# Kernel tuning notes

Hardware: AMD Instinct MI355X
Metric: run time of the kernel (lower is better)

Reference implementation:

```python
import jax, jax.numpy as jnp
import numpy as np

BITS = 4
GROUPSIZE = 128
INF = 4096
OUTF = 4096
PACK = 32 // BITS  # 8 nibbles per int32


def _dequant(qweight, qzeros, scales):
    # qweight: [INF//PACK, OUTF] int32, qzeros: [n_groups, OUTF//PACK] int32
    shifts = (jnp.arange(PACK, dtype=jnp.int32) * BITS)
    # unpack weights: each int32 row holds PACK consecutive input rows
    w = (qweight[:, None, :] >> shifts[None, :, None]) & 15        # [512, 8, 4096]
    w = w.reshape(-1, GROUPSIZE, OUTF)                              # [n_groups, groupsize, OUTF]
    # unpack zeros: each int32 col holds PACK consecutive output cols
    z = ((qzeros[:, :, None] >> shifts[None, None, :]) & 15) + 1   # [n_groups, 512, 8]
    z = z.reshape(z.shape[0], 1, -1)                                # [n_groups, 1, OUTF]
    W = scales[:, None, :] * (w - z).astype(scales.dtype)           # per-group dequant
    return W.reshape(INF, OUTF)


def setup_inputs() -> dict:
    key = jax.random.key(0)
    k1, k2, k3, k4, k5 = jax.random.split(key, 5)
    x = jax.random.normal(k1, (8, 512, INF), dtype=jnp.float32)
    qweight = jax.random.randint(k2, (INF // PACK, OUTF), 0, 2147483647, dtype=jnp.int32)
    n_groups = INF // GROUPSIZE
    qzeros = jax.random.randint(k3, (n_groups, OUTF // PACK), 0, 2147483647, dtype=jnp.int32)
    scales = jax.random.uniform(k4, (n_groups, OUTF), dtype=jnp.float32) * 0.01 + 0.001
    bias = jax.random.normal(k5, (OUTF,), dtype=jnp.float32) * 0.01
    return {"x": x, "qweight": qweight, "qzeros": qzeros, "scales": scales, "bias": bias}


def reference(x, qweight, qzeros, scales, bias):
    W = _dequant(qweight, qzeros, scales)        # [INF, OUTF] fp32
    out = jnp.matmul(x, W.astype(x.dtype)) + bias
    return out
```

## Files before the change

### kernel.cpp

```cpp
#include <hip/hip_runtime.h>
#include <hip/hip_bf16.h>


#define K_DIM 4096
#define N_DIM 4096
#define M_DIM 4096
#define BM 256
#define BN 256
#define BK 64
#define NGROUPS 32

typedef __attribute__((ext_vector_type(8))) short s8v;
typedef __attribute__((ext_vector_type(4))) float f4v;
typedef __attribute__((ext_vector_type(4))) unsigned int u4v;
typedef __attribute__((ext_vector_type(2))) unsigned int u2v;
typedef __attribute__((ext_vector_type(4))) float float4v;

typedef __attribute__((address_space(3))) void LDSV;
typedef const __attribute__((address_space(1))) void GLBV;

__device__ __forceinline__ void glds16(const void* g, void* l) {
    __builtin_amdgcn_global_load_lds((GLBV*)g, (LDSV*)l, 16, 0, 0);
}

__device__ __forceinline__ unsigned int bf16rne(float f) {
    unsigned int b = __float_as_uint(f);
    return (b + 0x7FFFu + ((b >> 16) & 1u)) >> 16;
}

__global__ __launch_bounds__(256) void castx(const float* __restrict__ x,
                                             unsigned short* __restrict__ xh,
                                             int n4) {
    int i0 = blockIdx.x * 256 + threadIdx.x;
    int st = gridDim.x * 256;
    for (int i = i0; i < n4; i += st) {
        float4v v = ((const float4v*)x)[i];
        unsigned int h[4];
#pragma unroll
        for (int j = 0; j < 4; j++) {
            unsigned int b = __float_as_uint(v[j]);
            h[j] = (b + 0x7FFFu + ((b >> 16) & 1u)) & 0xFFFF0000u;
        }
        u2v o = {(h[0] >> 16) | h[1], (h[2] >> 16) | h[3]};
        ((u2v*)xh)[i] = o;
    }
}

__global__ __launch_bounds__(256) void dequantW(const int* __restrict__ qw,
                                                const int* __restrict__ qz,
                                                const float* __restrict__ scales,
                                                unsigned short* __restrict__ wt) {
    __shared__ __align__(16) unsigned short T[256 * 64];
    const int b = blockIdx.x;
    const int kkb = b & 63;
    const int nb = b >> 6;
    const int tid = threadIdx.x;
    const int n = nb * 256 + tid;
    const int g = kkb >> 1;
    const float s = scales[g * N_DIM + n];
    const int zp1 = ((qz[g * 512 + (n >> 3)] >> ((n & 7) * 4)) & 15) + 1;

    char* Tb = (char*)T;
#pragma unroll
    for (int r = 0; r < 8; r++) {
        const unsigned int q = (unsigned int)qw[(kkb * 8 + r) * N_DIM + n];
        unsigned int hw[8];
#pragma unroll
        for (int j = 0; j < 8; j++) {
            float v = s * (float)((int)((q >> (4 * j)) & 15u) - zp1);
            hw[j] = bf16rne(v);
        }
        u4v d = {hw[0] | (hw[1] << 16), hw[2] | (hw[3] << 16),
                 hw[4] | (hw[5] << 16), hw[6] | (hw[7] << 16)};
        *(u4v*)(Tb + tid * 128 + ((r * 16) ^ ((tid & 7) << 4))) = d;
    }
    __syncthreads();
#pragma unroll
    for (int p = 0; p < 8; p++) {
        const int nl = p * 32 + (tid >> 3);
        const int c = tid & 7;
        u4v d = *(const u4v*)(Tb + nl * 128 + ((c * 16) ^ ((nl & 7) << 4)));
        *(u4v*)(wt + (size_t)(nb * 256 + nl) * K_DIM + kkb * 64 + c * 8) = d;
    }
}

#define STAGE_A(BUF, H, T)                                                    \
    {                                                                         \
        _Pragma("unroll") for (int j = 0; j < 2; j++) {                       \
            const int s_ = 2 * wid + j;                                       \
            const int rA = (s_ < 8) ? ((H) * 64 + s_ * 8)                     \
                                    : (128 + (H) * 64 + (s_ - 8) * 8);        \
            glds16(xh + (size_t)(bm + rA + (lane >> 3)) * K_DIM + (T)*BK +    \
                       aswz,                                                  \
                   &LDS_[BUF][0][(H)*8192 + s_ * 512]);                       \
        }                                                                     \
    }
#define STAGE_B(BUF, H, T)                                                    \
    {                                                                         \
        _Pragma("unroll") for (int j = 0; j < 2; j++) {                       \
            const int s_ = 2 * wid + j;                                       \
            const int cB = ((s_ >> 2) << 6) + ((H) << 5) + ((s_ & 3) << 3);   \
            glds16(wt + (size_t)(bn + cB + (lane >> 3)) * K_DIM + (T)*BK +    \
                       aswz,                                                  \
                   &LDS_[BUF][1][(H)*8192 + s_ * 512]);                       \
        }                                                                     \
    }
#define VM6 asm volatile("s_waitcnt vmcnt(6)" ::: "memory");
#define VM0 asm volatile("s_waitcnt vmcnt(0)" ::: "memory");
#define NOP ;

#define PHASE(BUF, QM, QN, STAGE_CODE, WAIT_CODE)                             \
    {                                                                         \
        if ((QN) == 0) {                                                      \
            const char* Ab = (const char*)&LDS_[BUF][0][(QM)*8192];           \
            _Pragma("unroll") for (int mi = 0; mi < 4; mi++) {                \
                const int pos = wr * 64 + mi * 16 + frow;                     \
                const int ro = pos * 128;                                     \
                const int sw = (pos & 7) << 4;                                \
                afr[mi][0] = *(const s8v*)(Ab + ro + (fk16 ^ sw));            \
                afr[mi][1] = *(const s8v*)(Ab + ro + ((64 | fk16) ^ sw));     \
            }                                                                 \
        }                                                                     \
        if ((QM) == 0) {                                                      \
            const char* Bb = (const char*)&LDS_[BUF][1][(QN)*8192];           \
            _Pragma("unroll") for (int ni = 0; ni < 2; ni++) {                \
                const int pos = wc * 32 + ni * 16 + frow;                     \
                const int ro = pos * 128;                                     \
                const int sw = (pos & 7) << 4;                                \
                bfr[QN][ni][0] = *(const s8v*)(Bb + ro + (fk16 ^ sw));        \
                bfr[QN][ni][1] = *(const s8v*)(Bb + ro + ((64 | fk16) ^ sw)); \
            }                                                                 \
        }                                                                     \
        STAGE_CODE                                                            \
        __builtin_amdgcn_s_barrier();                                         \
        asm volatile("s_waitcnt lgkmcnt(0)" ::: "memory");                    \
        __builtin_amdgcn_s_setprio(1);                                        \
        _Pragma("unroll") for (int mi = 0; mi < 4; mi++)                      \
            _Pragma("unroll") for (int ni = 0; ni < 2; ni++) {                \
            acc[(QM)*4 + mi][(QN)*2 + ni] =                                   \
                __builtin_amdgcn_mfma_f32_16x16x32_bf16(                      \
                    afr[mi][0], bfr[QN][ni][0],                               \
                    acc[(QM)*4 + mi][(QN)*2 + ni], 0, 0, 0);                  \
            acc[(QM)*4 + mi][(QN)*2 + ni] =                                   \
                __builtin_amdgcn_mfma_f32_16x16x32_bf16(                      \
                    afr[mi][1], bfr[QN][ni][1],                               \
                    acc[(QM)*4 + mi][(QN)*2 + ni], 0, 0, 0);                  \
        }                                                                     \
        __builtin_amdgcn_s_setprio(0);                                        \
        WAIT_CODE                                                             \
        __builtin_amdgcn_s_barrier();                                         \
    }

__global__ __launch_bounds__(512, 2) void gemm8(
    const unsigned short* __restrict__ xh, const unsigned short* __restrict__ wt,
    const float* __restrict__ bias, float* __restrict__ out) {
    __shared__ __align__(16) unsigned short LDS_[2][2][16384];

    const int tid = threadIdx.x;
    const int lane = tid & 63;
    const int wid = tid >> 6;
    const int wr = wid >> 2;
    const int wc = wid & 3;

    const int bid = blockIdx.x;
    const int wg = ((bid & 7) << 5) + (bid >> 3);
    const int bm = (wg >> 4) << 8;
    const int bn = (wg & 15) << 8;

    const int frow = lane & 15;
    const int fk16 = (lane >> 4) << 4;
    const int aswz = ((lane & 7) ^ (lane >> 3)) << 3;

    const f4v z4 = {0.f, 0.f, 0.f, 0.f};
    f4v acc[8][4];
#pragma unroll
    for (int i = 0; i < 8; i++)
#pragma unroll
        for (int j = 0; j < 4; j++) acc[i][j] = z4;

    s8v afr[4][2];
    s8v bfr[2][2][2];

    STAGE_A(0, 0, 0)
    STAGE_A(0, 1, 0)
    STAGE_B(0, 0, 0)
    STAGE_B(0, 1, 0)
    STAGE_A(1, 0, 1)
    STAGE_B(1, 0, 1)
    STAGE_B(1, 1, 1)
    VM6
    __builtin_amdgcn_s_barrier();

#pragma unroll 1
    for (int i = 0; i < 31; ++i) {
        const int t1 = 2 * i + 1, t2 = 2 * i + 2, t3 = 2 * i + 3;
        PHASE(0, 0, 0, STAGE_A(1, 1, t1), NOP)
        PHASE(0, 0, 1, STAGE_A(0, 0, t2), NOP)
        PHASE(0, 1, 0, STAGE_B(0, 0, t2), NOP)
        PHASE(0, 1, 1, STAGE_B(0, 1, t2), VM6)
        PHASE(1, 0, 0, STAGE_A(0, 1, t2), NOP)
        PHASE(1, 0, 1, STAGE_A(1, 0, t3), NOP)
        PHASE(1, 1, 0, STAGE_B(1, 0, t3), NOP)
        PHASE(1, 1, 1, STAGE_B(1, 1, t3), VM6)
    }
    PHASE(0, 0, 0, STAGE_A(1, 1, 63), NOP)
    PHASE(0, 0, 1, NOP, NOP)
    PHASE(0, 1, 0, NOP, NOP)
    PHASE(0, 1, 1, NOP, VM0)
    PHASE(1, 0, 0, NOP, NOP)
    PHASE(1, 0, 1, NOP, NOP)
    PHASE(1, 1, 0, NOP, NOP)
    PHASE(1, 1, 1, NOP, NOP)

    const int row0 = bm + wr * 128 + ((lane >> 4) << 2);
    const int col0 = bn + wc * 64 + frow;
#pragma unroll
    for (int n = 0; n < 4; n++) {
        const int cn = col0 + (n >> 1) * 32 + (n & 1) * 16;
        const float bv = bias[cn];
#pragma unroll
        for (int m = 0; m < 8; m++) {
            const int rm = row0 + (m >> 2) * 64 + (m & 3) * 16;
            f4v v = acc[m][n];
#pragma unroll
            for (int r2 = 0; r2 < 4; r2++)
                out[(size_t)(rm + r2) * N_DIM + cn] = v[r2] + bv;
        }
    }
}

__global__ __launch_bounds__(256) void naive_q4(
    const float* __restrict__ x, const int* __restrict__ qw,
    const int* __restrict__ qz, const float* __restrict__ scales,
    const float* __restrict__ bias, float* __restrict__ out) {
    const int n = (blockIdx.x & 63) * 64 + (threadIdx.x & 63);
    const int m = (blockIdx.x >> 6) * 4 + (threadIdx.x >> 6);
    const float* xr = x + (size_t)m * K_DIM;
    float acc = 0.f;
    for (int g = 0; g < NGROUPS; ++g) {
        const float s = scales[g * N_DIM + n];
        const int z = ((qz[g * 512 + (n >> 3)] >> ((n & 7) * 4)) & 15) + 1;
        float gs = 0.f;
        for (int kk = 0; kk < 16; ++kk) {
            const int q = qw[(g * 16 + kk) * N_DIM + n];
            const float* xp = xr + g * 128 + kk * 8;
#pragma unroll
            for (int j = 0; j < 8; j++)
                gs += xp[j] * (float)(((q >> (4 * j)) & 15) - z);
        }
        acc += s * gs;
    }
    out[(size_t)m * N_DIM + n] = acc + bias[n];
}

extern "C" void kernel_launch(void* const* d_in, const int* in_sizes, int n_in,
                              void* d_out, int out_size, void* d_ws,
                              size_t ws_size, hipStream_t stream) {
    const float* x = (const float*)d_in[0];
    const int* qw = (const int*)d_in[1];
    const int* qz = (const int*)d_in[2];
    const float* sc = (const float*)d_in[3];
    const float* bias = (const float*)d_in[4];
    float* out = (float*)d_out;

    const size_t nel = (size_t)M_DIM * K_DIM;
    const size_t need = nel * 2 * sizeof(unsigned short);
    if (ws_size >= need) {
        unsigned short* xh = (unsigned short*)d_ws;
        unsigned short* wtp = xh + nel;
        castx<<<2048, 256, 0, stream>>>(x, xh, (int)(nel / 4));
        dequantW<<<64 * 16, 256, 0, stream>>>(qw, qz, sc, wtp);
        gemm8<<<(M_DIM / BM) * (N_DIM / BN), 512, 0, stream>>>(xh, wtp, bias,
                                                               out);
    } else {
        naive_q4<<<(M_DIM / 4) * (N_DIM / 64), 256, 0, stream>>>(x, qw, qz, sc,
                                                                 bias, out);
    }
}
```

Before: 248.4 us.

## Fuse cast and dequant prep kernels; split GEMM phases to overlap LDS reads with MFMA

The x-to-bf16 cast and the weight dequantisation are merged into a single launch that gives them disjoint block ranges, saving one kernel launch and letting the two passes run at the same time. The GEMM main loop is rebuilt from 8 uniform phases into a per-buffer pass. A-fragment LDS reads are split into halves and interleaved with MFMA batches, so the second half's reads hide behind the first half's compute. This brings more barriers and scheduling changes that may perturb the compiler's instruction ordering and register pressure.

After: 246.2 us. Within noise of the previous version (-0.9%).

```diff
diff --git a/kernel.cpp b/kernel.cpp
--- a/kernel.cpp
+++ b/kernel.cpp
@@ -28,33 +28,34 @@
     return (b + 0x7FFFu + ((b >> 16) & 1u)) >> 16;
 }
 
-__global__ __launch_bounds__(256) void castx(const float* __restrict__ x,
-                                             unsigned short* __restrict__ xh,
-                                             int n4) {
-    int i0 = blockIdx.x * 256 + threadIdx.x;
-    int st = gridDim.x * 256;
-    for (int i = i0; i < n4; i += st) {
-        float4v v = ((const float4v*)x)[i];
-        unsigned int h[4];
-#pragma unroll
-        for (int j = 0; j < 4; j++) {
-            unsigned int b = __float_as_uint(v[j]);
-            h[j] = (b + 0x7FFFu + ((b >> 16) & 1u)) & 0xFFFF0000u;
-        }
-        u2v o = {(h[0] >> 16) | h[1], (h[2] >> 16) | h[3]};
-        ((u2v*)xh)[i] = o;
-    }
-}
-
-__global__ __launch_bounds__(256) void dequantW(const int* __restrict__ qw,
-                                                const int* __restrict__ qz,
-                                                const float* __restrict__ scales,
-                                                unsigned short* __restrict__ wt) {
+__global__ __launch_bounds__(256) void prep(const float* __restrict__ x,
+                                            unsigned short* __restrict__ xh,
+                                            const int* __restrict__ qw,
+                                            const int* __restrict__ qz,
+                                            const float* __restrict__ scales,
+                                            unsigned short* __restrict__ wt) {
     __shared__ __align__(16) unsigned short T[256 * 64];
+    const int tid = threadIdx.x;
+    if (blockIdx.x >= 1024) {
+        const int n4 = (M_DIM * K_DIM) / 4;
+        int i0 = (blockIdx.x - 1024) * 256 + tid;
+        const int st = 2048 * 256;
+        for (int i = i0; i < n4; i += st) {
+            float4v v = ((const float4v*)x)[i];
+            unsigned int h[4];
+#pragma unroll
+            for (int j = 0; j < 4; j++) {
+                unsigned int b = __float_as_uint(v[j]);
+                h[j] = (b + 0x7FFFu + ((b >> 16) & 1u)) & 0xFFFF0000u;
+            }
+            u2v o = {(h[0] >> 16) | h[1], (h[2] >> 16) | h[3]};
+            ((u2v*)xh)[i] = o;
+        }
+        return;
+    }
     const int b = blockIdx.x;
     const int kkb = b & 63;
     const int nb = b >> 6;
-    const int tid = threadIdx.x;
     const int n = nb * 256 + tid;
     const int g = kkb >> 1;
     const float s = scales[g * N_DIM + n];
@@ -105,51 +106,72 @@
                    &LDS_[BUF][1][(H)*8192 + s_ * 512]);                       \
         }                                                                     \
     }
+#define RD_A2(BUF, QM, MI0)                                                   \
+    {                                                                         \
+        const char* Ab = (const char*)&LDS_[BUF][0][(QM)*8192];               \
+        _Pragma("unroll") for (int mi = (MI0); mi < (MI0) + 2; mi++) {        \
+            const int pos = wr * 64 + mi * 16 + frow;                         \
+            const int ro = pos * 128;                                         \
+            const int sw = (pos & 7) << 4;                                    \
+            afr[mi][0] = *(const s8v*)(Ab + ro + (fk16 ^ sw));                \
+            afr[mi][1] = *(const s8v*)(Ab + ro + ((64 | fk16) ^ sw));         \
+        }                                                                     \
+    }
+#define RD_B(BUF, H)                                                          \
+    {                                                                         \
+        const char* Bb = (const char*)&LDS_[BUF][1][(H)*8192];                \
+        _Pragma("unroll") for (int ni = 0; ni < 2; ni++) {                    \
+            const int pos = wc * 32 + ni * 16 + frow;                         \
+            const int ro = pos * 128;                                         \
+            const int sw = (pos & 7) << 4;                                    \
+            bfr[H][ni][0] = *(const s8v*)(Bb + ro + (fk16 ^ sw));             \
+            bfr[H][ni][1] = *(const s8v*)(Bb + ro + ((64 | fk16) ^ sw));      \
+        }                                                                     \
+    }
+#define MM2(MI0, QM, QN)                                                      \
+    _Pragma("unroll") for (int mi = (MI0); mi < (MI0) + 2; mi++)              \
+        _Pragma("unroll") for (int ni = 0; ni < 2; ni++) {                    \
+        acc[(QM)*4 + mi][(QN)*2 + ni] =                                       \
+            __builtin_amdgcn_mfma_f32_16x16x32_bf16(                          \
+                afr[mi][0], bfr[QN][ni][0], acc[(QM)*4 + mi][(QN)*2 + ni], 0, \
+                0, 0);                                                        \
+        acc[(QM)*4 + mi][(QN)*2 + ni] =                                       \
+            __builtin_amdgcn_mfma_f32_16x16x32_bf16(                          \
+                afr[mi][1], bfr[QN][ni][1], acc[(QM)*4 + mi][(QN)*2 + ni], 0, \
+                0, 0);                                                        \
+    }
 #define VM6 asm volatile("s_waitcnt vmcnt(6)" ::: "memory");
 #define VM0 asm volatile("s_waitcnt vmcnt(0)" ::: "memory");
-#define NOP ;
-
-#define PHASE(BUF, QM, QN, STAGE_CODE, WAIT_CODE)                             \
-    {                                                                         \
-        if ((QN) == 0) {                                                      \
-            const char* Ab = (const char*)&LDS_[BUF][0][(QM)*8192];           \
-            _Pragma("unroll") for (int mi = 0; mi < 4; mi++) {                \
-                const int pos = wr * 64 + mi * 16 + frow;                     \
-                const int ro = pos * 128;                                     \
-                const int sw = (pos & 7) << 4;                                \
-                afr[mi][0] = *(const s8v*)(Ab + ro + (fk16 ^ sw));            \
-                afr[mi][1] = *(const s8v*)(Ab + ro + ((64 | fk16) ^ sw));     \
-            }                                                                 \
-        }                                                                     \
-        if ((QM) == 0) {                                                      \
-            const char* Bb = (const char*)&LDS_[BUF][1][(QN)*8192];           \
-            _Pragma("unroll") for (int ni = 0; ni < 2; ni++) {                \
-                const int pos = wc * 32 + ni * 16 + frow;                     \
-                const int ro = pos * 128;                                     \
-                const int sw = (pos & 7) << 4;                                \
-                bfr[QN][ni][0] = *(const s8v*)(Bb + ro + (fk16 ^ sw));        \
-                bfr[QN][ni][1] = *(const s8v*)(Bb + ro + ((64 | fk16) ^ sw)); \
-            }                                                                 \
-        }                                                                     \
-        STAGE_CODE                                                            \
-        __builtin_amdgcn_s_barrier();                                         \
-        asm volatile("s_waitcnt lgkmcnt(0)" ::: "memory");                    \
-        __builtin_amdgcn_s_setprio(1);                                        \
-        _Pragma("unroll") for (int mi = 0; mi < 4; mi++)                      \
-            _Pragma("unroll") for (int ni = 0; ni < 2; ni++) {                \
-            acc[(QM)*4 + mi][(QN)*2 + ni] =                                   \
-                __builtin_amdgcn_mfma_f32_16x16x32_bf16(                      \
-                    afr[mi][0], bfr[QN][ni][0],                               \
-                    acc[(QM)*4 + mi][(QN)*2 + ni], 0, 0, 0);                  \
-            acc[(QM)*4 + mi][(QN)*2 + ni] =                                   \
-                __builtin_amdgcn_mfma_f32_16x16x32_bf16(                      \
-                    afr[mi][1], bfr[QN][ni][1],                               \
-                    acc[(QM)*4 + mi][(QN)*2 + ni], 0, 0, 0);                  \
-        }                                                                     \
-        __builtin_amdgcn_s_setprio(0);                                        \
-        WAIT_CODE                                                             \
-        __builtin_amdgcn_s_barrier();                                         \
-    }
+#define BAR __builtin_amdgcn_s_barrier();
+#define PRIO1 __builtin_amdgcn_s_setprio(1);
+#define PRIO0 __builtin_amdgcn_s_setprio(0);
+
+#define BUFPASS(BUF, SC1, SC2, SC3, SC4, W4)                                  \
+    RD_A2(BUF, 0, 0) RD_B(BUF, 0)                                             \
+    SC1                                                                       \
+    BAR                                                                       \
+    PRIO1 MM2(0, 0, 0) PRIO0                                                  \
+    RD_A2(BUF, 0, 2) RD_B(BUF, 1)                                             \
+    PRIO1 MM2(2, 0, 0) PRIO0                                                  \
+    BAR                                                                       \
+    SC2                                                                       \
+    BAR                                                                       \
+    PRIO1 MM2(0, 0, 1) MM2(2, 0, 1) PRIO0                                     \
+    BAR                                                                       \
+    RD_A2(BUF, 1, 0)                                                          \
+    SC3                                                                       \
+    BAR                                                                       \
+    PRIO1 MM2(0, 1, 0) PRIO0                                                  \
+    RD_A2(BUF, 1, 2)                                                          \
+    PRIO1 MM2(2, 1, 0) PRIO0                                                  \
+    BAR                                                                       \
+    SC4                                                                       \
+    BAR                                                                       \
+    PRIO1 MM2(0, 1, 1) MM2(2, 1, 1) PRIO0                                     \
+    W4                                                                        \
+    BAR
+
+#define SNOP ;
 
 __global__ __launch_bounds__(512, 2) void gemm8(
     const unsigned short* __restrict__ xh, const unsigned short* __restrict__ wt,
@@ -189,28 +211,18 @@
     STAGE_B(1, 0, 1)
     STAGE_B(1, 1, 1)
     VM6
-    __builtin_amdgcn_s_barrier();
+    BAR
 
 #pragma unroll 1
     for (int i = 0; i < 31; ++i) {
         const int t1 = 2 * i + 1, t2 = 2 * i + 2, t3 = 2 * i + 3;
-        PHASE(0, 0, 0, STAGE_A(1, 1, t1), NOP)
-        PHASE(0, 0, 1, STAGE_A(0, 0, t2), NOP)
-        PHASE(0, 1, 0, STAGE_B(0, 0, t2), NOP)
-        PHASE(0, 1, 1, STAGE_B(0, 1, t2), VM6)
-        PHASE(1, 0, 0, STAGE_A(0, 1, t2), NOP)
-        PHASE(1, 0, 1, STAGE_A(1, 0, t3), NOP)
-        PHASE(1, 1, 0, STAGE_B(1, 0, t3), NOP)
-        PHASE(1, 1, 1, STAGE_B(1, 1, t3), VM6)
-    }
-    PHASE(0, 0, 0, STAGE_A(1, 1, 63), NOP)
-    PHASE(0, 0, 1, NOP, NOP)
-    PHASE(0, 1, 0, NOP, NOP)
-    PHASE(0, 1, 1, NOP, VM0)
-    PHASE(1, 0, 0, NOP, NOP)
-    PHASE(1, 0, 1, NOP, NOP)
-    PHASE(1, 1, 0, NOP, NOP)
-    PHASE(1, 1, 1, NOP, NOP)
+        BUFPASS(0, STAGE_A(1, 1, t1), STAGE_A(0, 0, t2), STAGE_B(0, 0, t2),
+                STAGE_B(0, 1, t2), VM6)
+        BUFPASS(1, STAGE_A(0, 1, t2), STAGE_A(1, 0, t3), STAGE_B(1, 0, t3),
+                STAGE_B(1, 1, t3), VM6)
+    }
+    BUFPASS(0, STAGE_A(1, 1, 63), SNOP, SNOP, SNOP, VM0)
+    BUFPASS(1, SNOP, SNOP, SNOP, SNOP, SNOP)
 
     const int row0 = bm + wr * 128 + ((lane >> 4) << 2);
     const int col0 = bn + wc * 64 + frow;
@@ -268,8 +280,7 @@
     if (ws_size >= need) {
         unsigned short* xh = (unsigned short*)d_ws;
         unsigned short* wtp = xh + nel;
-        castx<<<2048, 256, 0, stream>>>(x, xh, (int)(nel / 4));
-        dequantW<<<64 * 16, 256, 0, stream>>>(qw, qz, sc, wtp);
+        prep<<<3072, 256, 0, stream>>>(x, xh, qw, qz, sc, wtp);
         gemm8<<<(M_DIM / BM) * (N_DIM / BN), 512, 0, stream>>>(xh, wtp, bias,
                                                                out);
     } else {
```
